# Optimization experiments

Hardware: AMD Instinct MI355X
Metric: run time of the kernel (lower is better)

Reference implementation:

```python
import jax, jax.numpy as jnp
import numpy as np

N = 50000      # nodes
E = 600000     # edges
F_IN = 128     # num_features
H = 128        # hidden_dim

def setup_inputs() -> dict:
    key = jax.random.key(0)
    k1, k2, k3 = jax.random.split(key, 3)
    x = jax.random.normal(k1, (N, F_IN), dtype=jnp.float32)
    W = jax.random.normal(k2, (F_IN, H), dtype=jnp.float32) * 0.05
    b = jnp.zeros((H,), dtype=jnp.float32)
    edge_index = jax.random.randint(k3, (2, E), 0, N, dtype=jnp.int64)
    return {"x": x, "W": W, "b": b, "edge_index": edge_index}

def reference(x, W, b, edge_index):
    # GCNConv (PyG default): add self-loops, symmetric deg^-1/2 normalization,
    # out[t] = sum_{(s,t) in E'} norm(s,t) * (x @ W)[s] + b, then relu.
    n = x.shape[0]
    loops = jnp.arange(n, dtype=edge_index.dtype)
    src = jnp.concatenate([edge_index[0], loops])  # [E+N]
    dst = jnp.concatenate([edge_index[1], loops])  # [E+N]
    xw = x @ W                                      # [N, H]
    deg = jax.ops.segment_sum(jnp.ones_like(dst, dtype=xw.dtype), dst,
                              num_segments=n)       # [N], >=1 due to self-loops
    dinv = jax.lax.rsqrt(deg)
    norm = dinv[src] * dinv[dst]                    # [E+N]
    msg = xw[src] * norm[:, None]                   # [E+N, H] gather
    agg = jax.ops.segment_sum(msg, dst, num_segments=n)  # [N, H] scatter-add
    out = jax.nn.relu(agg + b)
    # F.dropout(training=False) is identity in eval mode.
    return out
```

## Files before the change

kernel.cpp:

```cpp
#include <hip/hip_runtime.h>
#include <stdint.h>


#define FDIM 128
#define HDIM 128
#define SCAN_CHUNK 1024

using s8v   = __attribute__((ext_vector_type(8))) short;
using f32x4 = __attribute__((ext_vector_type(4))) float;

__device__ __forceinline__ unsigned bf16rn(float f) {
    unsigned u = __float_as_uint(f);
    return (u + 0x7fffu + ((u >> 16) & 1u)) >> 16;
}
__device__ __forceinline__ void upfma(unsigned w, float ds, float& lo, float& hi) {
    lo = fmaf(ds, __uint_as_float(w << 16), lo);
    hi = fmaf(ds, __uint_as_float(w & 0xffff0000u), hi);
}

__global__ __launch_bounds__(256) void k_setup(int* __restrict__ deg,
                                               const float* __restrict__ W,
                                               uint4* __restrict__ Warr,
                                               int n, int packW) {
    const int i = blockIdx.x * 256 + threadIdx.x;
    if (i < n) deg[i] = 0;
    if (packW && i < (FDIM / 8) * HDIM) {
        const int chunk = i >> 7, nn = i & 127;
        float v[8];
#pragma unroll
        for (int j = 0; j < 8; ++j) v[j] = W[(chunk * 8 + j) * HDIM + nn];
        uint4 o;
        o.x = bf16rn(v[0]) | (bf16rn(v[1]) << 16);
        o.y = bf16rn(v[2]) | (bf16rn(v[3]) << 16);
        o.z = bf16rn(v[4]) | (bf16rn(v[5]) << 16);
        o.w = bf16rn(v[6]) | (bf16rn(v[7]) << 16);
        Warr[i] = o;
    }
}

__global__ __launch_bounds__(256) void k_count_xcast(const int* __restrict__ dst,
                                                     int* __restrict__ deg,
                                                     int* __restrict__ slot,
                                                     const float* __restrict__ x,
                                                     uint4* __restrict__ xb,
                                                     int e, int n, int fillBlocks) {
    if ((int)blockIdx.x < fillBlocks) {
        const int i = blockIdx.x * 256 + threadIdx.x;
        if (i < e) slot[i] = atomicAdd(&deg[dst[i]], 1);
    } else if (xb) {
        const long long idx = (long long)(blockIdx.x - fillBlocks) * 256 + threadIdx.x;
        if (idx >= (long long)n * (FDIM / 8)) return;
        const float4* xp = (const float4*)x + idx * 2;
        const float4 a = xp[0], b = xp[1];
        uint4 o;
        o.x = bf16rn(a.x) | (bf16rn(a.y) << 16);
        o.y = bf16rn(a.z) | (bf16rn(a.w) << 16);
        o.z = bf16rn(b.x) | (bf16rn(b.y) << 16);
        o.w = bf16rn(b.z) | (bf16rn(b.w) << 16);
        xb[idx] = o;
    }
}

__global__ __launch_bounds__(256) void k_scan1(const int* __restrict__ deg,
                                               int* __restrict__ rowptr,
                                               int* __restrict__ partials,
                                               float* __restrict__ dinv, int n) {
    __shared__ int sdata[256];
    const int tid = threadIdx.x;
    const int base = blockIdx.x * SCAN_CHUNK + tid * 4;
    int v[4];
    int s = 0;
#pragma unroll
    for (int j = 0; j < 4; ++j) {
        int idx = base + j;
        v[j] = (idx < n) ? deg[idx] : 0;
        if (idx < n) dinv[idx] = rsqrtf((float)v[j] + 1.0f);
        s += v[j];
    }
    sdata[tid] = s;
    __syncthreads();
    for (int off = 1; off < 256; off <<= 1) {
        int t = (tid >= off) ? sdata[tid - off] : 0;
        __syncthreads();
        sdata[tid] += t;
        __syncthreads();
    }
    int run = sdata[tid] - s;
#pragma unroll
    for (int j = 0; j < 4; ++j) {
        int idx = base + j;
        if (idx < n) rowptr[idx] = run;
        run += v[j];
    }
    if (tid == 255) partials[blockIdx.x] = sdata[255];
}

__global__ __launch_bounds__(256) void k_scan23(int* __restrict__ rowptr,
                                                const int* __restrict__ partials,
                                                int n, int e) {
    const int i = blockIdx.x * 256 + threadIdx.x;
    const int nb = blockIdx.x >> 2;
    int s = 0;
    for (int k = 0; k < nb; ++k) s += partials[k];
    if (i < n) rowptr[i] += s;
    if (i == n) rowptr[n] = e;
}

__global__ __launch_bounds__(256) void k_fill(const int* __restrict__ src,
                                              const int* __restrict__ dst,
                                              const int* __restrict__ slot,
                                              const int* __restrict__ rowptr,
                                              int* __restrict__ elist, int e) {
    int i = blockIdx.x * 256 + threadIdx.x;
    if (i < e) elist[rowptr[dst[i]] + slot[i]] = src[i];
}

__global__ __launch_bounds__(256) void k_gather_gemm(
    const uint4* __restrict__ xb, const float* __restrict__ dinv,
    const int* __restrict__ rowptr, const int* __restrict__ elist,
    const uint4* __restrict__ Warr, const float* __restrict__ bias,
    float* __restrict__ out, int n) {
    __shared__ uint4 zlds[16][16];
    const int tid = threadIdx.x;
    const int r = tid >> 4, q = tid & 15;
    const int node = blockIdx.x * 16 + r;
    const int wave = tid >> 6, lane = tid & 63;
    const int l16 = lane & 15, lg = lane >> 4;

    int beg = 0, end = 0;
    float di = 0.0f;
    if (node < n) {
        beg = rowptr[node];
        end = rowptr[node + 1];
        di = dinv[node];
    }

    s8v wf[2][4];
#pragma unroll
    for (int ntl = 0; ntl < 2; ++ntl)
#pragma unroll
        for (int ks = 0; ks < 4; ++ks)
            wf[ntl][ks] = *(const s8v*)&Warr[(ks * 4 + lg) * 128 +
                                             (wave * 2 + ntl) * 16 + l16];
    const float bv0 = bias[(wave * 2 + 0) * 16 + l16];
    const float bv1 = bias[(wave * 2 + 1) * 16 + l16];

    if (node < n) {
        const uint4* xq = xb + q;
        float a0 = 0.f, a1 = 0.f, a2 = 0.f, a3 = 0.f,
              a4 = 0.f, a5 = 0.f, a6 = 0.f, a7 = 0.f;
        {
            const uint4 v = xq[(size_t)node * 16];
            upfma(v.x, di, a0, a1); upfma(v.y, di, a2, a3);
            upfma(v.z, di, a4, a5); upfma(v.w, di, a6, a7);
        }
        for (int j = beg; j < end; j += 4) {
            const int i1 = (j + 1 < end) ? j + 1 : end - 1;
            const int i2 = (j + 2 < end) ? j + 2 : end - 1;
            const int i3 = (j + 3 < end) ? j + 3 : end - 1;
            const int s0 = elist[j], s1 = elist[i1];
            const int s2 = elist[i2], s3 = elist[i3];
            const float d0 = dinv[s0];
            const float d1 = (j + 1 < end) ? dinv[s1] : 0.0f;
            const float d2 = (j + 2 < end) ? dinv[s2] : 0.0f;
            const float d3 = (j + 3 < end) ? dinv[s3] : 0.0f;
            const uint4 u0 = xq[(size_t)s0 * 16];
            const uint4 u1 = xq[(size_t)s1 * 16];
            const uint4 u2 = xq[(size_t)s2 * 16];
            const uint4 u3 = xq[(size_t)s3 * 16];
            upfma(u0.x, d0, a0, a1); upfma(u0.y, d0, a2, a3);
            upfma(u0.z, d0, a4, a5); upfma(u0.w, d0, a6, a7);
            upfma(u1.x, d1, a0, a1); upfma(u1.y, d1, a2, a3);
            upfma(u1.z, d1, a4, a5); upfma(u1.w, d1, a6, a7);
            upfma(u2.x, d2, a0, a1); upfma(u2.y, d2, a2, a3);
            upfma(u2.z, d2, a4, a5); upfma(u2.w, d2, a6, a7);
            upfma(u3.x, d3, a0, a1); upfma(u3.y, d3, a2, a3);
            upfma(u3.z, d3, a4, a5); upfma(u3.w, d3, a6, a7);
        }
        uint4 o;
        o.x = bf16rn(a0 * di) | (bf16rn(a1 * di) << 16);
        o.y = bf16rn(a2 * di) | (bf16rn(a3 * di) << 16);
        o.z = bf16rn(a4 * di) | (bf16rn(a5 * di) << 16);
        o.w = bf16rn(a6 * di) | (bf16rn(a7 * di) << 16);
        zlds[r][q ^ r] = o;
    }
    __syncthreads();

    s8v afr[4];
#pragma unroll
    for (int ks = 0; ks < 4; ++ks)
        afr[ks] = *(const s8v*)&zlds[l16][(ks * 4 + lg) ^ l16];

#pragma unroll
    for (int ntl = 0; ntl < 2; ++ntl) {
        f32x4 acc = (f32x4){0.f, 0.f, 0.f, 0.f};
#pragma unroll
        for (int ks = 0; ks < 4; ++ks)
            acc = __builtin_amdgcn_mfma_f32_16x16x32_bf16(afr[ks], wf[ntl][ks], acc, 0, 0, 0);
        const int col = (wave * 2 + ntl) * 16 + l16;
        const float bv = ntl ? bv1 : bv0;
#pragma unroll
        for (int rr = 0; rr < 4; ++rr) {
            const int row = blockIdx.x * 16 + lg * 4 + rr;
            if (row < n)
                __builtin_nontemporal_store(fmaxf(acc[rr] + bv, 0.0f),
                                            &out[(size_t)row * HDIM + col]);
        }
    }
}

__global__ __launch_bounds__(256) void k_gather_f32(const float* __restrict__ x,
                                                    const float* __restrict__ dinv,
                                                    const int* __restrict__ rowptr,
                                                    const int* __restrict__ elist,
                                                    float* __restrict__ z, int n) {
    const int lane = threadIdx.x & 31;
    const int node = blockIdx.x * 8 + (threadIdx.x >> 5);
    if (node >= n) return;
    const float di = dinv[node];
    float4 v = ((const float4*)(x + (size_t)node * FDIM))[lane];
    float4 sum;
    sum.x = di * v.x; sum.y = di * v.y; sum.z = di * v.z; sum.w = di * v.w;
    const int beg = rowptr[node], end = rowptr[node + 1];
    for (int j = beg; j < end; ++j) {
        const int s = elist[j];
        const float ds = dinv[s];
        const float4 u = ((const float4*)(x + (size_t)s * FDIM))[lane];
        sum.x = fmaf(ds, u.x, sum.x);
        sum.y = fmaf(ds, u.y, sum.y);
        sum.z = fmaf(ds, u.z, sum.z);
        sum.w = fmaf(ds, u.w, sum.w);
    }
    float4 o;
    o.x = di * sum.x; o.y = di * sum.y; o.z = di * sum.z; o.w = di * sum.w;
    ((float4*)(z + (size_t)node * FDIM))[lane] = o;
}

__global__ __launch_bounds__(512) void k_gemm_relu(const float* __restrict__ W,
                                                   const float* __restrict__ bias,
                                                   float* __restrict__ zo, int n) {
    __shared__ float Wl[FDIM * HDIM];
    __shared__ float xs[4][FDIM];
    const int t = threadIdx.x;
    const int h = t & (HDIM - 1);
    const int g = t >> 7;
    {
        const float4* W4 = (const float4*)W;
        float4* Wl4 = (float4*)Wl;
        for (int i = t; i < FDIM * HDIM / 4; i += 512) Wl4[i] = W4[i];
    }
    __syncthreads();
    const float bv = bias[h];
    const int nq = (n + 3) >> 2;
    for (int q = blockIdx.x; q < nq; q += gridDim.x) {
        const int row = q * 4 + g;
        if (row < n) xs[g][h] = zo[(size_t)row * HDIM + h];
        __syncthreads();
        if (row < n) {
            float acc = bv;
#pragma unroll
            for (int k = 0; k < FDIM; ++k)
                acc = fmaf(xs[g][k], Wl[k * HDIM + h], acc);
            zo[(size_t)row * HDIM + h] = fmaxf(acc, 0.0f);
        }
        __syncthreads();
    }
}

extern "C" void kernel_launch(void* const* d_in, const int* in_sizes, int n_in,
                              void* d_out, int out_size, void* d_ws, size_t ws_size,
                              hipStream_t stream) {
    const float* x = (const float*)d_in[0];
    const float* W = (const float*)d_in[1];
    const float* b = (const float*)d_in[2];
    const int* ei = (const int*)d_in[3];
    float* out = (float*)d_out;

    const int H = in_sizes[2];
    const int F = in_sizes[1] / H;
    const int N = in_sizes[0] / F;
    const int E = in_sizes[3] / 2;
    const int* srcp = ei;
    const int* dstp = ei + E;

    auto align256 = [](size_t v) { return (v + 255) & ~(size_t)255; };
    char* ws = (char*)d_ws;
    size_t off = 0;
    int* deg = (int*)(ws + off);      off += align256((size_t)N * 4);
    float* dinv = (float*)(ws + off); off += align256((size_t)N * 4);
    int* rowptr = (int*)(ws + off);   off += align256((size_t)(N + 1) * 4);
    int* slot = (int*)(ws + off);     off += align256((size_t)E * 4);
    int* partials = (int*)(ws + off); off += 256;
    int* elist = (int*)(ws + off);    off += align256((size_t)E * 4);
    uint4* xb = (uint4*)(ws + off);   off += align256((size_t)N * FDIM * 2);
    uint4* Warr = (uint4*)(ws + off); off += align256((size_t)(FDIM / 8) * HDIM * 16);
    const bool fast = (ws_size >= off);

    const int nblk_scan = (N + SCAN_CHUNK - 1) / SCAN_CHUNK;
    const int fillBlocks = (E + 255) / 256;

    k_setup<<<(N + 255) / 256, 256, 0, stream>>>(deg, W, fast ? Warr : nullptr,
                                                 N, fast ? 1 : 0);
    if (fast) {
        const long long nchunks = (long long)N * (FDIM / 8);
        const int castBlocks = (int)((nchunks + 255) / 256);
        k_count_xcast<<<fillBlocks + castBlocks, 256, 0, stream>>>(
            dstp, deg, slot, x, xb, E, N, fillBlocks);
    } else {
        k_count_xcast<<<fillBlocks, 256, 0, stream>>>(dstp, deg, slot, x, nullptr,
                                                      E, N, fillBlocks);
    }
    k_scan1<<<nblk_scan, 256, 0, stream>>>(deg, rowptr, partials, dinv, N);
    k_scan23<<<(N + 1 + 255) / 256, 256, 0, stream>>>(rowptr, partials, N, E);
    k_fill<<<fillBlocks, 256, 0, stream>>>(srcp, dstp, slot, rowptr, elist, E);
    if (fast) {
        k_gather_gemm<<<(N + 15) / 16, 256, 0, stream>>>(xb, dinv, rowptr, elist,
                                                         Warr, b, out, N);
    } else {
        k_gather_f32<<<(N + 7) / 8, 256, 0, stream>>>(x, dinv, rowptr, elist, out, N);
        k_gemm_relu<<<512, 512, 0, stream>>>(W, b, out, N);
    }
}
```

Measured before the change: 88.20 us.

## Replace scan fixup pass with chunk offsets applied lazily; widen gather unroll

Removes the k_scan23 pass that rewrote every rowptr entry. A tiny single-wave k_scan2 now scans the per-chunk partials, and consumers add coff[node>>10] when reading rowptr. The gather loop is unrolled from 4 to 8 neighbors to raise memory-level parallelism, and the W/bias fragment loads move after the gather to reduce register pressure during it. Nontemporal loads are added for streamed edge arrays. Risks: k_scan2 assumes at most 64 chunks (N=50000 gives 49), and the extra coff lookups on every rowptr access.

```diff
diff --git a/kernel.cpp b/kernel.cpp
--- a/kernel.cpp
+++ b/kernel.cpp
@@ -46,7 +46,7 @@
                                                      int e, int n, int fillBlocks) {
     if ((int)blockIdx.x < fillBlocks) {
         const int i = blockIdx.x * 256 + threadIdx.x;
-        if (i < e) slot[i] = atomicAdd(&deg[dst[i]], 1);
+        if (i < e) slot[i] = atomicAdd(&deg[__builtin_nontemporal_load(dst + i)], 1);
     } else if (xb) {
         const long long idx = (long long)(blockIdx.x - fillBlocks) * 256 + threadIdx.x;
         if (idx >= (long long)n * (FDIM / 8)) return;
@@ -92,34 +92,42 @@
         if (idx < n) rowptr[idx] = run;
         run += v[j];
     }
-    if (tid == 255) partials[blockIdx.x] = sdata[255];
-}
-
-__global__ __launch_bounds__(256) void k_scan23(int* __restrict__ rowptr,
-                                                const int* __restrict__ partials,
-                                                int n, int e) {
-    const int i = blockIdx.x * 256 + threadIdx.x;
-    const int nb = blockIdx.x >> 2;
-    int s = 0;
-    for (int k = 0; k < nb; ++k) s += partials[k];
-    if (i < n) rowptr[i] += s;
-    if (i == n) rowptr[n] = e;
+    if (tid == 255) {
+        partials[blockIdx.x] = sdata[255];
+        if (blockIdx.x == (int)gridDim.x - 1) rowptr[n] = sdata[255];
+    }
+}
+
+__global__ __launch_bounds__(64) void k_scan2(int* __restrict__ partials, int nb) {
+    int l = threadIdx.x;
+    int v = (l < nb) ? partials[l] : 0;
+    int inc = v;
+    for (int off = 1; off < 64; off <<= 1) {
+        int t = __shfl_up(inc, off);
+        if (l >= off) inc += t;
+    }
+    if (l < nb) partials[l] = inc - v;
 }
 
 __global__ __launch_bounds__(256) void k_fill(const int* __restrict__ src,
                                               const int* __restrict__ dst,
                                               const int* __restrict__ slot,
                                               const int* __restrict__ rowptr,
+                                              const int* __restrict__ coff,
                                               int* __restrict__ elist, int e) {
     int i = blockIdx.x * 256 + threadIdx.x;
-    if (i < e) elist[rowptr[dst[i]] + slot[i]] = src[i];
+    if (i < e) {
+        const int d = __builtin_nontemporal_load(dst + i);
+        const int sl = __builtin_nontemporal_load(slot + i);
+        elist[rowptr[d] + coff[d >> 10] + sl] = __builtin_nontemporal_load(src + i);
+    }
 }
 
 __global__ __launch_bounds__(256) void k_gather_gemm(
     const uint4* __restrict__ xb, const float* __restrict__ dinv,
-    const int* __restrict__ rowptr, const int* __restrict__ elist,
-    const uint4* __restrict__ Warr, const float* __restrict__ bias,
-    float* __restrict__ out, int n) {
+    const int* __restrict__ rowptr, const int* __restrict__ coff,
+    const int* __restrict__ elist, const uint4* __restrict__ Warr,
+    const float* __restrict__ bias, float* __restrict__ out, int n) {
     __shared__ uint4 zlds[16][16];
     const int tid = threadIdx.x;
     const int r = tid >> 4, q = tid & 15;
@@ -127,25 +135,12 @@
     const int wave = tid >> 6, lane = tid & 63;
     const int l16 = lane & 15, lg = lane >> 4;
 
-    int beg = 0, end = 0;
-    float di = 0.0f;
     if (node < n) {
-        beg = rowptr[node];
-        end = rowptr[node + 1];
-        di = dinv[node];
-    }
-
-    s8v wf[2][4];
-#pragma unroll
-    for (int ntl = 0; ntl < 2; ++ntl)
-#pragma unroll
-        for (int ks = 0; ks < 4; ++ks)
-            wf[ntl][ks] = *(const s8v*)&Warr[(ks * 4 + lg) * 128 +
-                                             (wave * 2 + ntl) * 16 + l16];
-    const float bv0 = bias[(wave * 2 + 0) * 16 + l16];
-    const float bv1 = bias[(wave * 2 + 1) * 16 + l16];
-
-    if (node < n) {
+        const int co = coff[node >> 10];
+        const int beg = rowptr[node] + co;
+        const int end = rowptr[node + 1] + coff[(node + 1) >> 10];
+        const float di = dinv[node];
+
         const uint4* xq = xb + q;
         float a0 = 0.f, a1 = 0.f, a2 = 0.f, a3 = 0.f,
               a4 = 0.f, a5 = 0.f, a6 = 0.f, a7 = 0.f;
@@ -154,28 +149,24 @@
             upfma(v.x, di, a0, a1); upfma(v.y, di, a2, a3);
             upfma(v.z, di, a4, a5); upfma(v.w, di, a6, a7);
         }
-        for (int j = beg; j < end; j += 4) {
-            const int i1 = (j + 1 < end) ? j + 1 : end - 1;
-            const int i2 = (j + 2 < end) ? j + 2 : end - 1;
-            const int i3 = (j + 3 < end) ? j + 3 : end - 1;
-            const int s0 = elist[j], s1 = elist[i1];
-            const int s2 = elist[i2], s3 = elist[i3];
-            const float d0 = dinv[s0];
-            const float d1 = (j + 1 < end) ? dinv[s1] : 0.0f;
-            const float d2 = (j + 2 < end) ? dinv[s2] : 0.0f;
-            const float d3 = (j + 3 < end) ? dinv[s3] : 0.0f;
-            const uint4 u0 = xq[(size_t)s0 * 16];
-            const uint4 u1 = xq[(size_t)s1 * 16];
-            const uint4 u2 = xq[(size_t)s2 * 16];
-            const uint4 u3 = xq[(size_t)s3 * 16];
-            upfma(u0.x, d0, a0, a1); upfma(u0.y, d0, a2, a3);
-            upfma(u0.z, d0, a4, a5); upfma(u0.w, d0, a6, a7);
-            upfma(u1.x, d1, a0, a1); upfma(u1.y, d1, a2, a3);
-            upfma(u1.z, d1, a4, a5); upfma(u1.w, d1, a6, a7);
-            upfma(u2.x, d2, a0, a1); upfma(u2.y, d2, a2, a3);
-            upfma(u2.z, d2, a4, a5); upfma(u2.w, d2, a6, a7);
-            upfma(u3.x, d3, a0, a1); upfma(u3.y, d3, a2, a3);
-            upfma(u3.z, d3, a4, a5); upfma(u3.w, d3, a6, a7);
+        for (int j = beg; j < end; j += 8) {
+            int sidx[8];
+            float dw[8];
+#pragma unroll
+            for (int k = 0; k < 8; ++k) {
+                const int jj = j + k;
+                const int ii = (jj < end) ? jj : end - 1;
+                sidx[k] = __builtin_nontemporal_load(elist + ii);
+                dw[k] = (jj < end) ? dinv[sidx[k]] : 0.0f;
+            }
+            uint4 u[8];
+#pragma unroll
+            for (int k = 0; k < 8; ++k) u[k] = xq[(size_t)sidx[k] * 16];
+#pragma unroll
+            for (int k = 0; k < 8; ++k) {
+                upfma(u[k].x, dw[k], a0, a1); upfma(u[k].y, dw[k], a2, a3);
+                upfma(u[k].z, dw[k], a4, a5); upfma(u[k].w, dw[k], a6, a7);
+            }
         }
         uint4 o;
         o.x = bf16rn(a0 * di) | (bf16rn(a1 * di) << 16);
@@ -186,6 +177,16 @@
     }
     __syncthreads();
 
+    s8v wf[2][4];
+#pragma unroll
+    for (int ntl = 0; ntl < 2; ++ntl)
+#pragma unroll
+        for (int ks = 0; ks < 4; ++ks)
+            wf[ntl][ks] = *(const s8v*)&Warr[(ks * 4 + lg) * 128 +
+                                             (wave * 2 + ntl) * 16 + l16];
+    const float bv0 = bias[(wave * 2 + 0) * 16 + l16];
+    const float bv1 = bias[(wave * 2 + 1) * 16 + l16];
+
     s8v afr[4];
 #pragma unroll
     for (int ks = 0; ks < 4; ++ks)
@@ -212,6 +213,7 @@
 __global__ __launch_bounds__(256) void k_gather_f32(const float* __restrict__ x,
                                                     const float* __restrict__ dinv,
                                                     const int* __restrict__ rowptr,
+                                                    const int* __restrict__ coff,
                                                     const int* __restrict__ elist,
                                                     float* __restrict__ z, int n) {
     const int lane = threadIdx.x & 31;
@@ -221,7 +223,8 @@
     float4 v = ((const float4*)(x + (size_t)node * FDIM))[lane];
     float4 sum;
     sum.x = di * v.x; sum.y = di * v.y; sum.z = di * v.z; sum.w = di * v.w;
-    const int beg = rowptr[node], end = rowptr[node + 1];
+    const int beg = rowptr[node] + coff[node >> 10];
+    const int end = rowptr[node + 1] + coff[(node + 1) >> 10];
     for (int j = beg; j < end; ++j) {
         const int s = elist[j];
         const float ds = dinv[s];
@@ -311,13 +314,14 @@
                                                       E, N, fillBlocks);
     }
     k_scan1<<<nblk_scan, 256, 0, stream>>>(deg, rowptr, partials, dinv, N);
-    k_scan23<<<(N + 1 + 255) / 256, 256, 0, stream>>>(rowptr, partials, N, E);
-    k_fill<<<fillBlocks, 256, 0, stream>>>(srcp, dstp, slot, rowptr, elist, E);
+    k_scan2<<<1, 64, 0, stream>>>(partials, nblk_scan);
+    k_fill<<<fillBlocks, 256, 0, stream>>>(srcp, dstp, slot, rowptr, partials, elist, E);
     if (fast) {
-        k_gather_gemm<<<(N + 15) / 16, 256, 0, stream>>>(xb, dinv, rowptr, elist,
-                                                         Warr, b, out, N);
+        k_gather_gemm<<<(N + 15) / 16, 256, 0, stream>>>(xb, dinv, rowptr, partials,
+                                                         elist, Warr, b, out, N);
     } else {
-        k_gather_f32<<<(N + 7) / 8, 256, 0, stream>>>(x, dinv, rowptr, elist, out, N);
+        k_gather_f32<<<(N + 7) / 8, 256, 0, stream>>>(x, dinv, rowptr, partials,
+                                                      elist, out, N);
         k_gemm_relu<<<512, 512, 0, stream>>>(W, b, out, N);
     }
 }
```

New measurement: 106.5 us. 20.7% more time.
